# Optimization experiments

Measured on AMD Instinct MI355X. Metric: run time of the kernel, lower is better.

## Reference

```python
import jax, jax.numpy as jnp
import numpy as np

N_NODES = 100000
N_EDGES = 1600000
IN_DIM = 128
HID_DIM = 128
OUT_DIM = 64


def setup_inputs() -> dict:
    key = jax.random.key(0)
    k = jax.random.split(key, 6)
    x = jax.random.normal(k[0], (N_NODES, IN_DIM), dtype=jnp.float32)
    edge_index = jax.random.randint(k[1], (2, N_EDGES), 0, N_NODES, dtype=jnp.int32)
    # Glorot-ish init for GCNConv weights, zero bias (PyG default)
    W1 = jax.random.normal(k[2], (IN_DIM, HID_DIM), dtype=jnp.float32) * (1.0 / np.sqrt(IN_DIM))
    b1 = jnp.zeros((HID_DIM,), dtype=jnp.float32)
    W2 = jax.random.normal(k[3], (HID_DIM, OUT_DIM), dtype=jnp.float32) * (1.0 / np.sqrt(HID_DIM))
    b2 = jnp.zeros((OUT_DIM,), dtype=jnp.float32)
    return {"x": x, "edge_index": edge_index, "W1": W1, "b1": b1, "W2": W2, "b2": b2}


def _gcn_conv(x, src, dst, norm, W, b):
    # PyG GCNConv: linear transform, then symmetric-normalized aggregation over
    # edges (with self-loops already appended), then bias.
    h = x @ W                                   # [N, out]
    msg = h[src] * norm[:, None]                # [E+N, out] gather (irregular)
    out = jax.ops.segment_sum(msg, dst, num_segments=N_NODES)  # scatter-add at targets
    return out + b


def _build_norm(edge_index, dtype):
    loops = jnp.arange(N_NODES, dtype=edge_index.dtype)
    src = jnp.concatenate([edge_index[0], loops])  # source nodes j
    dst = jnp.concatenate([edge_index[1], loops])  # target nodes i
    deg = jax.ops.segment_sum(jnp.ones_like(dst, dtype=dtype), dst, num_segments=N_NODES)
    dinv = jnp.where(deg > 0, jax.lax.rsqrt(jnp.maximum(deg, 1e-12)), 0.0).astype(dtype)
    norm = dinv[src] * dinv[dst]
    return src, dst, norm


def reference(x, edge_index, W1, b1, W2, b2):
    src, dst, norm = _build_norm(edge_index, x.dtype)
    h = jax.nn.relu(_gcn_conv(x, src, dst, norm, W1, b1))
    return _gcn_conv(h, src, dst, norm, W2, b2)
```

## Files before the change

### kernel.cpp

```cpp
#include <hip/hip_runtime.h>


constexpr int N  = 100000;
constexpr int E  = 1600000;
constexpr int NB = (N + 255) / 256;
constexpr int CAP = 56;
constexpr int EB = (E + 255) / 256;
constexpr int CB = (N * 16 + 255) / 256;

typedef unsigned short u16;
typedef __attribute__((ext_vector_type(8))) short bf16x8;
typedef __attribute__((ext_vector_type(4))) float f32x4;


__device__ __forceinline__ unsigned bf16rne(float f) {
  unsigned u = __float_as_uint(f);
  return (u + 0x7fffu + ((u >> 16) & 1u)) >> 16;
}
__device__ __forceinline__ unsigned pk(float lo, float hi) {
  return bf16rne(lo) | (bf16rne(hi) << 16);
}
__device__ __forceinline__ void acc8(float (&a)[8], const uint4& u, float wgt) {
  a[0] = fmaf(wgt, __uint_as_float(u.x << 16), a[0]);
  a[1] = fmaf(wgt, __uint_as_float(u.x & 0xffff0000u), a[1]);
  a[2] = fmaf(wgt, __uint_as_float(u.y << 16), a[2]);
  a[3] = fmaf(wgt, __uint_as_float(u.y & 0xffff0000u), a[3]);
  a[4] = fmaf(wgt, __uint_as_float(u.z << 16), a[4]);
  a[5] = fmaf(wgt, __uint_as_float(u.z & 0xffff0000u), a[5]);
  a[6] = fmaf(wgt, __uint_as_float(u.w << 16), a[6]);
  a[7] = fmaf(wgt, __uint_as_float(u.w & 0xffff0000u), a[7]);
}


__global__ __launch_bounds__(256) void k_count_conv(
    const int* __restrict__ dst, int* __restrict__ counts, int* __restrict__ rank,
    const float* __restrict__ x, uint4* __restrict__ xb) {
  int b = blockIdx.x;
  if (b < EB) {
    int e = b * 256 + threadIdx.x;
    if (e < E) rank[e] = atomicAdd(&counts[dst[e]], 1);
  } else {
    int i = (b - EB) * 256 + threadIdx.x;
    if (i >= N * 16) return;
    const float4* x4 = reinterpret_cast<const float4*>(x);
    float4 v0 = x4[(size_t)i * 2];
    float4 v1 = x4[(size_t)i * 2 + 1];
    uint4 o;
    o.x = pk(v0.x, v0.y);
    o.y = pk(v0.z, v0.w);
    o.z = pk(v1.x, v1.y);
    o.w = pk(v1.z, v1.w);
    xb[i] = o;
  }
}

__global__ void k_finish(const int* __restrict__ counts, float* __restrict__ dinv) {
  int i = blockIdx.x * 256 + threadIdx.x;
  if (i < N) dinv[i] = rsqrtf((float)(counts[i] + 1));
}


__global__ __launch_bounds__(256) void k_fill(
    const int* __restrict__ src, const int* __restrict__ dst,
    const int* __restrict__ rank, int* __restrict__ col) {
  int e = blockIdx.x * 256 + threadIdx.x;
  if (e < E) col[(size_t)dst[e] * CAP + rank[e]] = src[e];
}


__global__ __launch_bounds__(256) void k_wprep(
    const float* __restrict__ W1, const float* __restrict__ W2,
    uint4* __restrict__ Wb1, uint4* __restrict__ Wb2) {
  int t = blockIdx.x * 256 + threadIdx.x;
  if (t < 2048) {
    int ct = t >> 8, kc = (t >> 6) & 3, l = t & 63;
    int k0 = kc * 32 + (l >> 4) * 8;
    int c = ct * 16 + (l & 15);
    uint4 o;
    o.x = pk(W1[(k0 + 0) * 128 + c], W1[(k0 + 1) * 128 + c]);
    o.y = pk(W1[(k0 + 2) * 128 + c], W1[(k0 + 3) * 128 + c]);
    o.z = pk(W1[(k0 + 4) * 128 + c], W1[(k0 + 5) * 128 + c]);
    o.w = pk(W1[(k0 + 6) * 128 + c], W1[(k0 + 7) * 128 + c]);
    Wb1[t] = o;
  } else if (t < 3072) {
    int u = t - 2048;
    int ct = u >> 8, kc = (u >> 6) & 3, l = u & 63;
    int k0 = kc * 32 + (l >> 4) * 8;
    int c = ct * 16 + (l & 15);
    uint4 o;
    o.x = pk(W2[(k0 + 0) * 64 + c], W2[(k0 + 1) * 64 + c]);
    o.y = pk(W2[(k0 + 2) * 64 + c], W2[(k0 + 3) * 64 + c]);
    o.z = pk(W2[(k0 + 4) * 64 + c], W2[(k0 + 5) * 64 + c]);
    o.w = pk(W2[(k0 + 6) * 64 + c], W2[(k0 + 7) * 64 + c]);
    Wb2[u] = o;
  }
}


template <int DIM, bool SRC_W, bool BIAS, bool OUT_BF16>
__global__ __launch_bounds__(256) void k_agg(
    const uint4* __restrict__ t, const int* __restrict__ counts,
    const int* __restrict__ col, const float* __restrict__ dinv,
    const float* __restrict__ bias, void* __restrict__ out) {
  constexpr int L = DIM / 8;
  constexpr int NPB = 256 / L;
  const int node = blockIdx.x * NPB + threadIdx.x / L;
  const int lane = threadIdx.x % L;
  if (node >= N) return;
  const size_t s0 = (size_t)node * CAP;
  const int cnt = counts[node];
  const float di = dinv[node];

  float a[8] = {0, 0, 0, 0, 0, 0, 0, 0};
  acc8(a, t[(size_t)node * L + lane], SRC_W ? di : 1.0f);
  for (int e = 0; e < cnt; e += 4) {
    const int last = cnt - 1;
    int sA = col[s0 + e];
    int sB = col[s0 + min(e + 1, last)];
    int sC = col[s0 + min(e + 2, last)];
    int sD = col[s0 + min(e + 3, last)];
    float wA, wB, wC, wD;
    if (SRC_W) {
      wA = rsqrtf((float)(counts[sA] + 1));
      wB = (e + 1 <= last) ? rsqrtf((float)(counts[sB] + 1)) : 0.0f;
      wC = (e + 2 <= last) ? rsqrtf((float)(counts[sC] + 1)) : 0.0f;
      wD = (e + 3 <= last) ? rsqrtf((float)(counts[sD] + 1)) : 0.0f;
    } else {
      wA = 1.0f;
      wB = (e + 1 <= last) ? 1.0f : 0.0f;
      wC = (e + 2 <= last) ? 1.0f : 0.0f;
      wD = (e + 3 <= last) ? 1.0f : 0.0f;
    }
    uint4 vA = t[(size_t)sA * L + lane];
    uint4 vB = t[(size_t)sB * L + lane];
    uint4 vC = t[(size_t)sC * L + lane];
    uint4 vD = t[(size_t)sD * L + lane];
    acc8(a, vA, wA);
    acc8(a, vB, wB);
    acc8(a, vC, wC);
    acc8(a, vD, wD);
  }
  if (OUT_BF16) {
    uint4 o;
    o.x = pk(di * a[0], di * a[1]);
    o.y = pk(di * a[2], di * a[3]);
    o.z = pk(di * a[4], di * a[5]);
    o.w = pk(di * a[6], di * a[7]);
    reinterpret_cast<uint4*>(out)[(size_t)node * L + lane] = o;
  } else {
    float4 r0 = {di * a[0], di * a[1], di * a[2], di * a[3]};
    float4 r1 = {di * a[4], di * a[5], di * a[6], di * a[7]};
    if (BIAS) {
      const float4* b4 = reinterpret_cast<const float4*>(bias) + lane * 2;
      float4 b0 = b4[0], b1 = b4[1];
      r0.x += b0.x; r0.y += b0.y; r0.z += b0.z; r0.w += b0.w;
      r1.x += b1.x; r1.y += b1.y; r1.z += b1.z; r1.w += b1.w;
    }
    float4* o4 = reinterpret_cast<float4*>(out) + (size_t)node * (DIM / 4) + lane * 2;
    o4[0] = r0;
    o4[1] = r1;
  }
}


template <int OUTC, bool EPI1>
__global__ __launch_bounds__(256, 1) void k_gemm_mfma(
    const u16* __restrict__ A, const uint4* __restrict__ Wsw,
    const float* __restrict__ bias, const float* __restrict__ dinv,
    u16* __restrict__ out) {
  constexpr int CT = OUTC / 16;
  const int lane = threadIdx.x & 63;
  const int lr = lane & 15;
  const int lk = lane >> 4;
  const int gw = blockIdx.x * 4 + (threadIdx.x >> 6);
  const int nw = gridDim.x * 4;
  const bf16x8* Wf = reinterpret_cast<const bf16x8*>(Wsw);

  bf16x8 b[CT][4];
  #pragma unroll
  for (int ct = 0; ct < CT; ++ct)
    #pragma unroll
    for (int kc = 0; kc < 4; ++kc)
      b[ct][kc] = Wf[(ct * 4 + kc) * 64 + lane];

  float bl[CT];
  if (EPI1) {
    #pragma unroll
    for (int ct = 0; ct < CT; ++ct) bl[ct] = bias[ct * 16 + lr];
  }

  const f32x4 fz = {0.f, 0.f, 0.f, 0.f};
  for (int s = gw; s < N / 16; s += nw) {
    const u16* ar = A + (size_t)(s * 16 + lr) * 128 + lk * 8;
    bf16x8 a[4];
    #pragma unroll
    for (int kc = 0; kc < 4; ++kc)
      a[kc] = *reinterpret_cast<const bf16x8*>(ar + kc * 32);
    f32x4 acc[CT];
    #pragma unroll
    for (int ct = 0; ct < CT; ++ct) acc[ct] = fz;
    #pragma unroll
    for (int kc = 0; kc < 4; ++kc)
      #pragma unroll
      for (int ct = 0; ct < CT; ++ct)
        acc[ct] = __builtin_amdgcn_mfma_f32_16x16x32_bf16(a[kc], b[ct][kc],
                                                          acc[ct], 0, 0, 0);
    const int rbase = s * 16 + lk * 4;
    float dv[4];
    if (EPI1) {
      #pragma unroll
      for (int ri = 0; ri < 4; ++ri) dv[ri] = dinv[rbase + ri];
    }
    #pragma unroll
    for (int ct = 0; ct < CT; ++ct) {
      const int c = ct * 16 + lr;
      #pragma unroll
      for (int ri = 0; ri < 4; ++ri) {
        float v = acc[ct][ri];
        if (EPI1) v = fmaxf(v + bl[ct], 0.f) * dv[ri];
        out[(size_t)(rbase + ri) * OUTC + c] = (u16)bf16rne(v);
      }
    }
  }
}


extern "C" void kernel_launch(void* const* d_in, const int* in_sizes, int n_in,
                              void* d_out, int out_size, void* d_ws, size_t ws_size,
                              hipStream_t stream) {
  const float* x  = (const float*)d_in[0];
  const int*   ei = (const int*)d_in[1];
  const float* W1 = (const float*)d_in[2];
  const float* b1 = (const float*)d_in[3];
  const float* W2 = (const float*)d_in[4];
  const float* b2 = (const float*)d_in[5];
  float* out = (float*)d_out;
  const int* src = ei;
  const int* dst = ei + E;

  char* p = (char*)d_ws;
  auto alloc = [&](size_t bytes) {
    void* q = p;
    p += (bytes + 255) & ~size_t(255);
    return q;
  };
  int*   counts = (int*)alloc((size_t)N * 4);
  int*   rank   = (int*)alloc((size_t)E * 4);
  int*   col    = (int*)alloc((size_t)N * CAP * 4);
  float* dinv   = (float*)alloc((size_t)N * 4);
  uint4* xb     = (uint4*)alloc((size_t)N * 256);
  uint4* xa     = (uint4*)alloc((size_t)N * 256);
  uint4* Wb1    = (uint4*)alloc(2048 * 16);
  uint4* Wb2    = (uint4*)alloc(1024 * 16);

  (void)hipMemsetAsync(counts, 0, (size_t)N * 4, stream);
  k_wprep<<<12, 256, 0, stream>>>(W1, W2, Wb1, Wb2);
  k_count_conv<<<EB + CB, 256, 0, stream>>>(dst, counts, rank, x, xb);
  k_finish<<<NB, 256, 0, stream>>>(counts, dinv);
  k_fill<<<EB, 256, 0, stream>>>(src, dst, rank, col);

  k_agg<128, true, false, true><<<(N + 15) / 16, 256, 0, stream>>>(
      xb, counts, col, dinv, nullptr, xa);
  k_gemm_mfma<128, true><<<512, 256, 0, stream>>>(
      (const u16*)xa, Wb1, b1, dinv, (u16*)xb);

  k_gemm_mfma<64, false><<<512, 256, 0, stream>>>(
      (const u16*)xb, Wb2, nullptr, nullptr, (u16*)xa);
  k_agg<64, false, true, false><<<(N + 31) / 32, 256, 0, stream>>>(
      xa, counts, col, dinv, b2, out);
}
```

Measured before the change: 234.0 us.

## Fuse layer-1 aggregation with both MFMA GEMMs in one kernel via LDS

Layer-1 neighbor aggregation, the W1 GEMM with bias/ReLU/normalization epilogue, and the W2 GEMM now run in a single kernel. Each 16-node tile is staged through shared memory, which removes the global-memory round trips of the intermediate feature buffers and two kernel launches. The separate dinv kernel is dropped and degree normalization is recomputed on the fly from counts. Aggregation loops now use a remainder loop instead of clamped duplicate loads. The trade-off is that the GEMM weights are reloaded per block and the tile is synchronized twice.

```diff
diff --git a/kernel.cpp b/kernel.cpp
--- a/kernel.cpp
+++ b/kernel.cpp
@@ -3,7 +3,6 @@
 
 constexpr int N  = 100000;
 constexpr int E  = 1600000;
-constexpr int NB = (N + 255) / 256;
 constexpr int CAP = 56;
 constexpr int EB = (E + 255) / 256;
 constexpr int CB = (N * 16 + 255) / 256;
@@ -54,11 +53,6 @@
   }
 }
 
-__global__ void k_finish(const int* __restrict__ counts, float* __restrict__ dinv) {
-  int i = blockIdx.x * 256 + threadIdx.x;
-  if (i < N) dinv[i] = rsqrtf((float)(counts[i] + 1));
-}
-
 
 __global__ __launch_bounds__(256) void k_fill(
     const int* __restrict__ src, const int* __restrict__ dst,
@@ -97,131 +91,157 @@
 }
 
 
-template <int DIM, bool SRC_W, bool BIAS, bool OUT_BF16>
-__global__ __launch_bounds__(256) void k_agg(
+__global__ __launch_bounds__(256) void k_layer1(
+    const uint4* __restrict__ xb, const int* __restrict__ counts,
+    const int* __restrict__ col, const float* __restrict__ b1,
+    const uint4* __restrict__ Wb1, const uint4* __restrict__ Wb2,
+    u16* __restrict__ xa2) {
+  __shared__ u16 lds_a[16][136];
+  __shared__ u16 lds_h[16][136];
+  __shared__ float lds_di[16];
+  const int tid = threadIdx.x;
+  const int nodeBase = blockIdx.x * 16;
+
+  {
+    const int n = tid >> 4;
+    const int d8 = tid & 15;
+    const int node = nodeBase + n;
+    const int cnt = counts[node];
+    const float wself = rsqrtf((float)(cnt + 1));
+    if (d8 == 0) lds_di[n] = wself;
+    const size_t s0 = (size_t)node * CAP;
+
+    float a[8] = {0, 0, 0, 0, 0, 0, 0, 0};
+    acc8(a, xb[(size_t)node * 16 + d8], wself);
+    int e = 0;
+    for (; e + 4 <= cnt; e += 4) {
+      int sA = col[s0 + e];
+      int sB = col[s0 + e + 1];
+      int sC = col[s0 + e + 2];
+      int sD = col[s0 + e + 3];
+      float wA = rsqrtf((float)(counts[sA] + 1));
+      float wB = rsqrtf((float)(counts[sB] + 1));
+      float wC = rsqrtf((float)(counts[sC] + 1));
+      float wD = rsqrtf((float)(counts[sD] + 1));
+      uint4 vA = xb[(size_t)sA * 16 + d8];
+      uint4 vB = xb[(size_t)sB * 16 + d8];
+      uint4 vC = xb[(size_t)sC * 16 + d8];
+      uint4 vD = xb[(size_t)sD * 16 + d8];
+      acc8(a, vA, wA);
+      acc8(a, vB, wB);
+      acc8(a, vC, wC);
+      acc8(a, vD, wD);
+    }
+    for (; e < cnt; ++e) {
+      int s = col[s0 + e];
+      float w = rsqrtf((float)(counts[s] + 1));
+      acc8(a, xb[(size_t)s * 16 + d8], w);
+    }
+    uint4 o;
+    o.x = pk(a[0], a[1]);
+    o.y = pk(a[2], a[3]);
+    o.z = pk(a[4], a[5]);
+    o.w = pk(a[6], a[7]);
+    *reinterpret_cast<uint4*>(&lds_a[n][d8 * 8]) = o;
+  }
+  __syncthreads();
+
+  const int lane = tid & 63;
+  const int w = tid >> 6;
+  const int lr = lane & 15;
+  const int lk = lane >> 4;
+  const bf16x8* Wf1 = reinterpret_cast<const bf16x8*>(Wb1);
+  const bf16x8* Wf2 = reinterpret_cast<const bf16x8*>(Wb2);
+  const f32x4 fz = {0.f, 0.f, 0.f, 0.f};
+  {
+    bf16x8 af[4];
+    #pragma unroll
+    for (int kc = 0; kc < 4; ++kc)
+      af[kc] = *reinterpret_cast<const bf16x8*>(&lds_a[lr][kc * 32 + lk * 8]);
+    f32x4 acc1[2] = {fz, fz};
+    #pragma unroll
+    for (int kc = 0; kc < 4; ++kc) {
+      #pragma unroll
+      for (int i = 0; i < 2; ++i) {
+        bf16x8 bf = Wf1[((w * 2 + i) * 4 + kc) * 64 + lane];
+        acc1[i] = __builtin_amdgcn_mfma_f32_16x16x32_bf16(af[kc], bf, acc1[i], 0, 0, 0);
+      }
+    }
+    #pragma unroll
+    for (int i = 0; i < 2; ++i) {
+      const int c = (w * 2 + i) * 16 + lr;
+      const float bl = b1[c];
+      #pragma unroll
+      for (int ri = 0; ri < 4; ++ri) {
+        const int r = lk * 4 + ri;
+        const float di = lds_di[r];
+        float v = fmaxf(di * acc1[i][ri] + bl, 0.f) * di;
+        lds_h[r][c] = (u16)bf16rne(v);
+      }
+    }
+  }
+  __syncthreads();
+
+  {
+    bf16x8 a2[4];
+    #pragma unroll
+    for (int kc = 0; kc < 4; ++kc)
+      a2[kc] = *reinterpret_cast<const bf16x8*>(&lds_h[lr][kc * 32 + lk * 8]);
+    f32x4 acc2 = fz;
+    #pragma unroll
+    for (int kc = 0; kc < 4; ++kc) {
+      bf16x8 bf = Wf2[(w * 4 + kc) * 64 + lane];
+      acc2 = __builtin_amdgcn_mfma_f32_16x16x32_bf16(a2[kc], bf, acc2, 0, 0, 0);
+    }
+    #pragma unroll
+    for (int ri = 0; ri < 4; ++ri) {
+      const int row = nodeBase + lk * 4 + ri;
+      xa2[(size_t)row * 64 + w * 16 + lr] = (u16)bf16rne(acc2[ri]);
+    }
+  }
+}
+
+
+__global__ __launch_bounds__(256) void k_agg2(
     const uint4* __restrict__ t, const int* __restrict__ counts,
-    const int* __restrict__ col, const float* __restrict__ dinv,
-    const float* __restrict__ bias, void* __restrict__ out) {
-  constexpr int L = DIM / 8;
-  constexpr int NPB = 256 / L;
-  const int node = blockIdx.x * NPB + threadIdx.x / L;
-  const int lane = threadIdx.x % L;
+    const int* __restrict__ col, const float* __restrict__ bias,
+    float* __restrict__ out) {
+  const int node = blockIdx.x * 32 + (threadIdx.x >> 3);
+  const int lane = threadIdx.x & 7;
   if (node >= N) return;
   const size_t s0 = (size_t)node * CAP;
   const int cnt = counts[node];
-  const float di = dinv[node];
+  const float di = rsqrtf((float)(cnt + 1));
 
   float a[8] = {0, 0, 0, 0, 0, 0, 0, 0};
-  acc8(a, t[(size_t)node * L + lane], SRC_W ? di : 1.0f);
-  for (int e = 0; e < cnt; e += 4) {
-    const int last = cnt - 1;
+  acc8(a, t[(size_t)node * 8 + lane], 1.0f);
+  int e = 0;
+  for (; e + 4 <= cnt; e += 4) {
     int sA = col[s0 + e];
-    int sB = col[s0 + min(e + 1, last)];
-    int sC = col[s0 + min(e + 2, last)];
-    int sD = col[s0 + min(e + 3, last)];
-    float wA, wB, wC, wD;
-    if (SRC_W) {
-      wA = rsqrtf((float)(counts[sA] + 1));
-      wB = (e + 1 <= last) ? rsqrtf((float)(counts[sB] + 1)) : 0.0f;
-      wC = (e + 2 <= last) ? rsqrtf((float)(counts[sC] + 1)) : 0.0f;
-      wD = (e + 3 <= last) ? rsqrtf((float)(counts[sD] + 1)) : 0.0f;
-    } else {
-      wA = 1.0f;
-      wB = (e + 1 <= last) ? 1.0f : 0.0f;
-      wC = (e + 2 <= last) ? 1.0f : 0.0f;
-      wD = (e + 3 <= last) ? 1.0f : 0.0f;
-    }
-    uint4 vA = t[(size_t)sA * L + lane];
-    uint4 vB = t[(size_t)sB * L + lane];
-    uint4 vC = t[(size_t)sC * L + lane];
-    uint4 vD = t[(size_t)sD * L + lane];
-    acc8(a, vA, wA);
-    acc8(a, vB, wB);
-    acc8(a, vC, wC);
-    acc8(a, vD, wD);
-  }
-  if (OUT_BF16) {
-    uint4 o;
-    o.x = pk(di * a[0], di * a[1]);
-    o.y = pk(di * a[2], di * a[3]);
-    o.z = pk(di * a[4], di * a[5]);
-    o.w = pk(di * a[6], di * a[7]);
-    reinterpret_cast<uint4*>(out)[(size_t)node * L + lane] = o;
-  } else {
-    float4 r0 = {di * a[0], di * a[1], di * a[2], di * a[3]};
-    float4 r1 = {di * a[4], di * a[5], di * a[6], di * a[7]};
-    if (BIAS) {
-      const float4* b4 = reinterpret_cast<const float4*>(bias) + lane * 2;
-      float4 b0 = b4[0], b1 = b4[1];
-      r0.x += b0.x; r0.y += b0.y; r0.z += b0.z; r0.w += b0.w;
-      r1.x += b1.x; r1.y += b1.y; r1.z += b1.z; r1.w += b1.w;
-    }
-    float4* o4 = reinterpret_cast<float4*>(out) + (size_t)node * (DIM / 4) + lane * 2;
-    o4[0] = r0;
-    o4[1] = r1;
-  }
-}
-
-
-template <int OUTC, bool EPI1>
-__global__ __launch_bounds__(256, 1) void k_gemm_mfma(
-    const u16* __restrict__ A, const uint4* __restrict__ Wsw,
-    const float* __restrict__ bias, const float* __restrict__ dinv,
-    u16* __restrict__ out) {
-  constexpr int CT = OUTC / 16;
-  const int lane = threadIdx.x & 63;
-  const int lr = lane & 15;
-  const int lk = lane >> 4;
-  const int gw = blockIdx.x * 4 + (threadIdx.x >> 6);
-  const int nw = gridDim.x * 4;
-  const bf16x8* Wf = reinterpret_cast<const bf16x8*>(Wsw);
-
-  bf16x8 b[CT][4];
-  #pragma unroll
-  for (int ct = 0; ct < CT; ++ct)
-    #pragma unroll
-    for (int kc = 0; kc < 4; ++kc)
-      b[ct][kc] = Wf[(ct * 4 + kc) * 64 + lane];
-
-  float bl[CT];
-  if (EPI1) {
-    #pragma unroll
-    for (int ct = 0; ct < CT; ++ct) bl[ct] = bias[ct * 16 + lr];
-  }
-
-  const f32x4 fz = {0.f, 0.f, 0.f, 0.f};
-  for (int s = gw; s < N / 16; s += nw) {
-    const u16* ar = A + (size_t)(s * 16 + lr) * 128 + lk * 8;
-    bf16x8 a[4];
-    #pragma unroll
-    for (int kc = 0; kc < 4; ++kc)
-      a[kc] = *reinterpret_cast<const bf16x8*>(ar + kc * 32);
-    f32x4 acc[CT];
-    #pragma unroll
-    for (int ct = 0; ct < CT; ++ct) acc[ct] = fz;
-    #pragma unroll
-    for (int kc = 0; kc < 4; ++kc)
-      #pragma unroll
-      for (int ct = 0; ct < CT; ++ct)
-        acc[ct] = __builtin_amdgcn_mfma_f32_16x16x32_bf16(a[kc], b[ct][kc],
-                                                          acc[ct], 0, 0, 0);
-    const int rbase = s * 16 + lk * 4;
-    float dv[4];
-    if (EPI1) {
-      #pragma unroll
-      for (int ri = 0; ri < 4; ++ri) dv[ri] = dinv[rbase + ri];
-    }
-    #pragma unroll
-    for (int ct = 0; ct < CT; ++ct) {
-      const int c = ct * 16 + lr;
-      #pragma unroll
-      for (int ri = 0; ri < 4; ++ri) {
-        float v = acc[ct][ri];
-        if (EPI1) v = fmaxf(v + bl[ct], 0.f) * dv[ri];
-        out[(size_t)(rbase + ri) * OUTC + c] = (u16)bf16rne(v);
-      }
-    }
-  }
+    int sB = col[s0 + e + 1];
+    int sC = col[s0 + e + 2];
+    int sD = col[s0 + e + 3];
+    uint4 vA = t[(size_t)sA * 8 + lane];
+    uint4 vB = t[(size_t)sB * 8 + lane];
+    uint4 vC = t[(size_t)sC * 8 + lane];
+    uint4 vD = t[(size_t)sD * 8 + lane];
+    acc8(a, vA, 1.0f);
+    acc8(a, vB, 1.0f);
+    acc8(a, vC, 1.0f);
+    acc8(a, vD, 1.0f);
+  }
+  for (; e < cnt; ++e)
+    acc8(a, t[(size_t)col[s0 + e] * 8 + lane], 1.0f);
+
+  const float4* b4 = reinterpret_cast<const float4*>(bias) + lane * 2;
+  float4 b0 = b4[0], b1v = b4[1];
+  float4 r0 = {fmaf(di, a[0], b0.x), fmaf(di, a[1], b0.y),
+               fmaf(di, a[2], b0.z), fmaf(di, a[3], b0.w)};
+  float4 r1 = {fmaf(di, a[4], b1v.x), fmaf(di, a[5], b1v.y),
+               fmaf(di, a[6], b1v.z), fmaf(di, a[7], b1v.w)};
+  float4* o4 = reinterpret_cast<float4*>(out) + (size_t)node * 16 + lane * 2;
+  o4[0] = r0;
+  o4[1] = r1;
 }
 
 
@@ -247,25 +267,18 @@
   int*   counts = (int*)alloc((size_t)N * 4);
   int*   rank   = (int*)alloc((size_t)E * 4);
   int*   col    = (int*)alloc((size_t)N * CAP * 4);
-  float* dinv   = (float*)alloc((size_t)N * 4);
   uint4* xb     = (uint4*)alloc((size_t)N * 256);
-  uint4* xa     = (uint4*)alloc((size_t)N * 256);
+  u16*   xa2    = (u16*)alloc((size_t)N * 64 * 2);
   uint4* Wb1    = (uint4*)alloc(2048 * 16);
   uint4* Wb2    = (uint4*)alloc(1024 * 16);
 
   (void)hipMemsetAsync(counts, 0, (size_t)N * 4, stream);
   k_wprep<<<12, 256, 0, stream>>>(W1, W2, Wb1, Wb2);
   k_count_conv<<<EB + CB, 256, 0, stream>>>(dst, counts, rank, x, xb);
-  k_finish<<<NB, 256, 0, stream>>>(counts, dinv);
   k_fill<<<EB, 256, 0, stream>>>(src, dst, rank, col);
 
-  k_agg<128, true, false, true><<<(N + 15) / 16, 256, 0, stream>>>(
-      xb, counts, col, dinv, nullptr, xa);
-  k_gemm_mfma<128, true><<<512, 256, 0, stream>>>(
-      (const u16*)xa, Wb1, b1, dinv, (u16*)xb);
-
-  k_gemm_mfma<64, false><<<512, 256, 0, stream>>>(
-      (const u16*)xb, Wb2, nullptr, nullptr, (u16*)xa);
-  k_agg<64, false, true, false><<<(N + 31) / 32, 256, 0, stream>>>(
-      xa, counts, col, dinv, b2, out);
-}
+  k_layer1<<<N / 16, 256, 0, stream>>>(xb, counts, col, b1, Wb1, Wb2, xa2);
+
+  k_agg2<<<N / 32, 256, 0, stream>>>(
+      reinterpret_cast<const uint4*>(xa2), counts, col, b2, out);
+}
```

After: 208.7 us. -10.8%, faster.
